# Kernel optimization log

Hardware: AMD Instinct MI355X
Metric: run time of the kernel (lower is better)

The kernel has to match this reference:

```python
import jax, jax.numpy as jnp
import numpy as np

B, E, M, S, D, H = 32, 48, 96, 48, 256, 8  # docs, entities/doc, mentions/doc, sentences/doc, hidden, heads
NEG = -1e9


def _layer_norm(x, g, b, eps=1e-5):
    mu = jnp.mean(x, axis=-1, keepdims=True)
    var = jnp.mean((x - mu) ** 2, axis=-1, keepdims=True)
    return (x - mu) * jax.lax.rsqrt(var + eps) * g + b


def _mha(key_in, value_in, query_in, mask, W, b, ln):
    # W: [4, D, D] = (Wq, Wk, Wv, Wout); b: [4, D]; ln: [2, D] = (gamma, beta)
    Bq, Lq, _ = query_in.shape
    dph = D // H

    def proj(x, i):
        return (x @ W[i] + b[i]).reshape(Bq, -1, H, dph).transpose(0, 2, 1, 3)  # [B,H,L,dph]

    q = proj(query_in, 0)
    k = proj(key_in, 1)
    v = proj(value_in, 2)
    scores = jnp.einsum('bhqd,bhkd->bhqk', q, k) / jnp.sqrt(jnp.float32(dph))
    scores = jnp.where(mask[:, None, :, :], NEG, scores)  # mask True = mention not of this entity
    attn = jax.nn.softmax(scores, axis=-1)
    ctx = jnp.einsum('bhqk,bhkd->bhqd', attn, v).transpose(0, 2, 1, 3).reshape(Bq, Lq, D)
    out = ctx @ W[3] + b[3]
    return _layer_norm(query_in + out, ln[0], ln[1])  # residual + LayerNorm


def _forward(info, entities, mentions, sentences, W1, b1, ln1, W2, b2, ln2):
    # uniform sections -> split_n_pad is an exact reshape
    ent = entities.reshape(B, E, D)
    men = mentions.reshape(B, M, D)
    men_sen = sentences[info[:, 4]].reshape(B, M, D)  # F.embedding(info[:,4], sentences)
    eids = jnp.arange(B * E, dtype=info.dtype).reshape(B, E)  # eid_ranges split per doc
    m_ids = info[:, 0].reshape(B, M)
    index_m = m_ids[:, None, :] != eids[:, :, None]  # [B,E,M], True = masked out
    # head mask varies with row entity i; tail mask varies with column entity j
    mask_h = jnp.broadcast_to(index_m[:, :, None, :], (B, E, E, M)).reshape(B, E * E, M)
    mask_t = jnp.broadcast_to(index_m[:, None, :, :], (B, E, E, M)).reshape(B, E * E, M)
    # meshgrid gather: query_2[b,i,j] = ent[b,j] (c_idx), query_1[b,i,j] = ent[b,i] (r_idx)
    q2 = jnp.broadcast_to(ent[:, None, :, :], (B, E, E, D)).reshape(B, E * E, D)
    q1 = jnp.broadcast_to(ent[:, :, None, :], (B, E, E, D)).reshape(B, E * E, D)
    pair_h = _mha(men_sen, men, q2, mask_h, W1, b1, ln1)
    pair_t = _mha(men_sen, men, q1, mask_t, W2, b2, ln2)
    return pair_h, pair_t


def setup_inputs():
    key = jax.random.key(0)
    ks = jax.random.split(key, 6)
    entities = jax.random.normal(ks[0], (B * E, D), jnp.float32)
    mentions = jax.random.normal(ks[1], (B * M, D), jnp.float32)
    sentences = jax.random.normal(ks[2], (B * S, D), jnp.float32)
    rng = np.random.RandomState(0)
    doc = np.repeat(np.arange(B), M)
    # every entity gets at least one mention (first E mentions per doc), rest random
    eid_local = np.stack([np.concatenate([np.arange(E), rng.randint(0, E, M - E)]) for _ in range(B)]).reshape(-1)
    sid_local = rng.randint(0, S, B * M)
    info = np.zeros((B * M, 6), np.int64)
    info[:, 0] = doc * E + eid_local  # global entity id
    info[:, 4] = doc * S + sid_local  # global sentence id
    section = np.tile(np.array([[E, M]], dtype=np.int64), (B, 1))
    W1 = jax.random.normal(ks[3], (4, D, D), jnp.float32) * 0.05
    W2 = jax.random.normal(ks[4], (4, D, D), jnp.float32) * 0.05
    b1 = jnp.zeros((4, D), jnp.float32)
    b2 = jnp.zeros((4, D), jnp.float32)
    ln1 = jnp.stack([jnp.ones(D), jnp.zeros(D)]).astype(jnp.float32)
    ln2 = jnp.stack([jnp.ones(D), jnp.zeros(D)]).astype(jnp.float32)
    return dict(info=jnp.asarray(info), section=jnp.asarray(section), entities=entities,
                mentions=mentions, sentences=sentences, W1=W1, b1=b1, ln1=ln1, W2=W2, b2=b2, ln2=ln2)


def reference(info, section, entities, mentions, sentences, W1, b1, ln1, W2, b2, ln2):
    return _forward(info, entities, mentions, sentences, W1, b1, ln1, W2, b2, ln2)
```

## Files before the change

kernel.cpp:

```cpp
#include <hip/hip_runtime.h>

#define B_ 32
#define E_ 48
#define M_ 96
#define D_ 256
#define H_ 8
#define DPH_ 32
#define MAXL_ 16
#define JT_ 16
#define RT_ 16
#define RT2_ 8

__global__ __launch_bounds__(256) void build_lists_kernel(
    const int* __restrict__ info, int* __restrict__ cnt, int* __restrict__ lst) {
    int g = blockIdx.x * 256 + threadIdx.x;
    if (g >= B_ * M_) return;
    int e = info[g * 6];
    int pos = atomicAdd(&cnt[e], 1);
    if (pos < MAXL_) lst[e * MAXL_ + pos] = g % M_;
}

__global__ __launch_bounds__(256) void prep_kernel(
    const float* __restrict__ ent, const float* __restrict__ men,
    const float* __restrict__ sen, const int* __restrict__ info,
    const float* __restrict__ W1, const float* __restrict__ b1,
    const float* __restrict__ W2, const float* __restrict__ b2,
    float* __restrict__ qh, float* __restrict__ qt,
    float* __restrict__ k1, float* __restrict__ k2,
    float* __restrict__ u1, float* __restrict__ u2) {
    __shared__ float a[RT_][D_];
    int bx = blockIdx.x;
    int tid = threadIdx.x;
    int type, rg, mha;
    if (bx < 768) { type = 2; rg = bx >> 1; mha = bx & 1; }
    else if (bx < 1152) { type = 1; rg = (bx - 768) >> 1; mha = bx & 1; }
    else { type = 0; rg = (bx - 1152) >> 1; mha = bx & 1; }

    const float* Wb = mha ? W2 : W1;
    const float* bb = mha ? b2 : b1;
    const float* W = Wb + (size_t)type * D_ * D_;
    int tx = tid & 127, ty = tid >> 7;

    if (type == 2) {
        int rowbase = rg * RT2_;
        for (int r = 0; r < RT2_; ++r)
            a[r][tid] = men[(size_t)(rowbase + r) * D_ + tid];
        __syncthreads();

        int r0 = ty * 4;
        float acc0[4], acc1[4];
        {
            float bv0 = bb[2 * D_ + tx], bv1 = bb[2 * D_ + tx + 128];
#pragma unroll
            for (int i = 0; i < 4; ++i) { acc0[i] = bv0; acc1[i] = bv1; }
        }
        for (int k = 0; k < D_; k += 4) {
            float wA0 = W[(size_t)k * D_ + tx],       wB0 = W[(size_t)k * D_ + tx + 128];
            float wA1 = W[(size_t)(k + 1) * D_ + tx], wB1 = W[(size_t)(k + 1) * D_ + tx + 128];
            float wA2 = W[(size_t)(k + 2) * D_ + tx], wB2 = W[(size_t)(k + 2) * D_ + tx + 128];
            float wA3 = W[(size_t)(k + 3) * D_ + tx], wB3 = W[(size_t)(k + 3) * D_ + tx + 128];
#pragma unroll
            for (int i = 0; i < 4; ++i) {
                float4 av = *(const float4*)&a[r0 + i][k];
                acc0[i] = fmaf(av.x, wA0, acc0[i]); acc1[i] = fmaf(av.x, wB0, acc1[i]);
                acc0[i] = fmaf(av.y, wA1, acc0[i]); acc1[i] = fmaf(av.y, wB1, acc1[i]);
                acc0[i] = fmaf(av.z, wA2, acc0[i]); acc1[i] = fmaf(av.z, wB2, acc1[i]);
                acc0[i] = fmaf(av.w, wA3, acc0[i]); acc1[i] = fmaf(av.w, wB3, acc1[i]);
            }
        }
        __syncthreads();
#pragma unroll
        for (int i = 0; i < 4; ++i) {
            a[r0 + i][tx] = acc0[i];
            a[r0 + i][tx + 128] = acc1[i];
        }
        __syncthreads();
        const float* Wo = Wb + (size_t)3 * D_ * D_;
        float* u = mha ? u2 : u1;
        for (int h = 0; h < H_; ++h) {
#pragma unroll
            for (int i = 0; i < 4; ++i) { acc0[i] = 0.f; acc1[i] = 0.f; }
            for (int k = 0; k < DPH_; k += 4) {
                int kk = h * DPH_ + k;
                float wA0 = Wo[(size_t)kk * D_ + tx],       wB0 = Wo[(size_t)kk * D_ + tx + 128];
                float wA1 = Wo[(size_t)(kk + 1) * D_ + tx], wB1 = Wo[(size_t)(kk + 1) * D_ + tx + 128];
                float wA2 = Wo[(size_t)(kk + 2) * D_ + tx], wB2 = Wo[(size_t)(kk + 2) * D_ + tx + 128];
                float wA3 = Wo[(size_t)(kk + 3) * D_ + tx], wB3 = Wo[(size_t)(kk + 3) * D_ + tx + 128];
#pragma unroll
                for (int i = 0; i < 4; ++i) {
                    float4 vv = *(const float4*)&a[r0 + i][kk & 255];
                    acc0[i] = fmaf(vv.x, wA0, acc0[i]); acc1[i] = fmaf(vv.x, wB0, acc1[i]);
                    acc0[i] = fmaf(vv.y, wA1, acc0[i]); acc1[i] = fmaf(vv.y, wB1, acc1[i]);
                    acc0[i] = fmaf(vv.z, wA2, acc0[i]); acc1[i] = fmaf(vv.z, wB2, acc1[i]);
                    acc0[i] = fmaf(vv.w, wA3, acc0[i]); acc1[i] = fmaf(vv.w, wB3, acc1[i]);
                }
            }
#pragma unroll
            for (int i = 0; i < 4; ++i) {
                u[((size_t)(rowbase + r0 + i) * H_ + h) * D_ + tx] = acc0[i];
                u[((size_t)(rowbase + r0 + i) * H_ + h) * D_ + tx + 128] = acc1[i];
            }
        }
        return;
    }

    int rowbase = rg * RT_;
    if (type == 0) {
        for (int r = tid >> 7; r < RT_; r += 2)
            a[r][tid & 127] = ent[(size_t)(rowbase + r) * D_ + (tid & 127)];
        for (int r = tid >> 7; r < RT_; r += 2)
            a[r][(tid & 127) + 128] = ent[(size_t)(rowbase + r) * D_ + (tid & 127) + 128];
    } else {
        for (int r = 0; r < RT_; ++r) {
            int sid = info[(rowbase + r) * 6 + 4];
            a[r][tid] = sen[(size_t)sid * D_ + tid];
        }
    }
    __syncthreads();

    int r0 = ty * 8;
    float acc0[8], acc1[8];
    {
        float bv0 = bb[type * D_ + tx], bv1 = bb[type * D_ + tx + 128];
#pragma unroll
        for (int i = 0; i < 8; ++i) { acc0[i] = bv0; acc1[i] = bv1; }
    }
    for (int k = 0; k < D_; k += 4) {
        float wA0 = W[(size_t)k * D_ + tx],       wB0 = W[(size_t)k * D_ + tx + 128];
        float wA1 = W[(size_t)(k + 1) * D_ + tx], wB1 = W[(size_t)(k + 1) * D_ + tx + 128];
        float wA2 = W[(size_t)(k + 2) * D_ + tx], wB2 = W[(size_t)(k + 2) * D_ + tx + 128];
        float wA3 = W[(size_t)(k + 3) * D_ + tx], wB3 = W[(size_t)(k + 3) * D_ + tx + 128];
#pragma unroll
        for (int i = 0; i < 8; ++i) {
            float4 av = *(const float4*)&a[r0 + i][k];
            acc0[i] = fmaf(av.x, wA0, acc0[i]); acc1[i] = fmaf(av.x, wB0, acc1[i]);
            acc0[i] = fmaf(av.y, wA1, acc0[i]); acc1[i] = fmaf(av.y, wB1, acc1[i]);
            acc0[i] = fmaf(av.z, wA2, acc0[i]); acc1[i] = fmaf(av.z, wB2, acc1[i]);
            acc0[i] = fmaf(av.w, wA3, acc0[i]); acc1[i] = fmaf(av.w, wB3, acc1[i]);
        }
    }

    float* o = (type == 0) ? (mha ? qt : qh) : (mha ? k2 : k1);
#pragma unroll
    for (int i = 0; i < 8; ++i) {
        o[(size_t)(rowbase + r0 + i) * D_ + tx] = acc0[i];
        o[(size_t)(rowbase + r0 + i) * D_ + tx + 128] = acc1[i];
    }
}

__global__ __launch_bounds__(256) void scores_kernel(
    const float* __restrict__ qh, const float* __restrict__ qt,
    const float* __restrict__ k1, const float* __restrict__ k2,
    float* __restrict__ ES) {
    int b = blockIdx.x, h = blockIdx.y, which = blockIdx.z;
    int tid = threadIdx.x;
    const float* q = (which ? qt : qh) + (size_t)b * E_ * D_ + h * DPH_;
    const float* kk = (which ? k2 : k1) + (size_t)b * M_ * D_ + h * DPH_;
    float* ESb = ES + (((size_t)which * B_ + b) * H_ + h) * (M_ * E_);

    __shared__ float qs[E_][DPH_ + 2];
    __shared__ float ks[M_][DPH_ + 2];
    __shared__ float Sb[E_][M_ + 2];
    __shared__ float mx[E_];

    for (int idx = tid; idx < E_ * DPH_; idx += 256) {
        int r = idx >> 5, c = idx & 31;
        qs[r][c] = q[(size_t)r * D_ + c];
    }
    for (int idx = tid; idx < M_ * DPH_; idx += 256) {
        int r = idx >> 5, c = idx & 31;
        ks[r][c] = kk[(size_t)r * D_ + c];
    }
    __syncthreads();
#pragma unroll
    for (int it = 0; it < 18; ++it) {
        int pair = tid + it * 256;
        int qi = pair / 96, m = pair % 96;
        float acc = 0.f;
#pragma unroll
        for (int c = 0; c < DPH_; c += 2) {
            float2 qv = *(const float2*)&qs[qi][c];
            float2 kv = *(const float2*)&ks[m][c];
            acc = fmaf(qv.x, kv.x, acc);
            acc = fmaf(qv.y, kv.y, acc);
        }
        Sb[qi][m] = acc * 0.17677669529663687f;
    }
    __syncthreads();
    if (tid < E_) {
        float mm = -1e30f;
        for (int m = 0; m < M_; ++m) mm = fmaxf(mm, Sb[tid][m]);
        mx[tid] = mm;
    }
    __syncthreads();
    for (int idx = tid; idx < E_ * M_; idx += 256) {
        int qi = idx % E_, m = idx / E_;
        ESb[m * E_ + qi] = __expf(Sb[qi][m] - mx[qi]);
    }
}

__global__ __launch_bounds__(256) void pairs_kernel(
    const int* __restrict__ cnt_arr, const int* __restrict__ lst_arr,
    const float* __restrict__ ES,
    const float* __restrict__ u1, const float* __restrict__ u2,
    const float* __restrict__ ent,
    const float* __restrict__ bo1, const float* __restrict__ bo2,
    const float* __restrict__ ln1, const float* __restrict__ ln2,
    float* __restrict__ out) {
    int tid = threadIdx.x;
    int me = blockIdx.x;
    int b = blockIdx.y;
    int which = blockIdx.z;

    const float* ESb = ES + ((size_t)which * B_ + b) * (H_ * M_ * E_);
    const float* u = which ? u2 : u1;
    const float* bo = which ? bo2 : bo1;
    const float* ln = which ? ln2 : ln1;
    float* outb = out + ((size_t)which * B_ + b) * E_ * E_ * D_;

    __shared__ int lst[MAXL_];
    __shared__ float wj[MAXL_ * H_][JT_];
    __shared__ float dinv_s[H_ * JT_];
    __shared__ float xbuf[JT_][D_ + 4];
    __shared__ int cnt_s;

    if (tid == 0) cnt_s = min(cnt_arr[b * E_ + me], MAXL_);
    if (tid < MAXL_) lst[tid] = lst_arr[(b * E_ + me) * MAXL_ + tid];
    __syncthreads();
    int cnt = cnt_s;
    int K = cnt * H_;

    float bv = bo[tid];
    int wave = tid >> 6, lane = tid & 63;

    for (int j0 = 0; j0 < E_; j0 += JT_) {
        for (int idx = tid; idx < K * 4; idx += 256) {
            int k = idx >> 2, j4 = (idx & 3) * 4;
            int pos = k >> 3, h = k & 7;
            *(float4*)&wj[k][j4] =
                *(const float4*)&ESb[(size_t)(h * M_ + lst[pos]) * E_ + j0 + j4];
        }
        __syncthreads();
        if (tid < H_ * JT_) {
            int h = tid >> 4, j = tid & 15;
            float s = 0.f;
            for (int pos = 0; pos < cnt; ++pos) s += wj[pos * 8 + h][j];
            dinv_s[tid] = 1.0f / s;
        }
        __syncthreads();
        for (int idx = tid; idx < K * JT_; idx += 256) {
            int k = idx >> 4, j = idx & 15;
            wj[k][j] *= dinv_s[((k & 7) << 4) + j];
        }
        __syncthreads();

        float acc[JT_];
#pragma unroll
        for (int j = 0; j < JT_; ++j) acc[j] = 0.f;
        for (int pos = 0; pos < cnt; ++pos) {
            const float* ub = u + (size_t)(b * M_ + lst[pos]) * (H_ * D_) + tid;
#pragma unroll
            for (int h = 0; h < H_; ++h) {
                float uval = ub[(size_t)h * D_];
                const float* wb = wj[pos * 8 + h];
                float4 w0 = *(const float4*)&wb[0];
                float4 w1 = *(const float4*)&wb[4];
                float4 w2 = *(const float4*)&wb[8];
                float4 w3 = *(const float4*)&wb[12];
                acc[0]  = fmaf(w0.x, uval, acc[0]);
                acc[1]  = fmaf(w0.y, uval, acc[1]);
                acc[2]  = fmaf(w0.z, uval, acc[2]);
                acc[3]  = fmaf(w0.w, uval, acc[3]);
                acc[4]  = fmaf(w1.x, uval, acc[4]);
                acc[5]  = fmaf(w1.y, uval, acc[5]);
                acc[6]  = fmaf(w1.z, uval, acc[6]);
                acc[7]  = fmaf(w1.w, uval, acc[7]);
                acc[8]  = fmaf(w2.x, uval, acc[8]);
                acc[9]  = fmaf(w2.y, uval, acc[9]);
                acc[10] = fmaf(w2.z, uval, acc[10]);
                acc[11] = fmaf(w2.w, uval, acc[11]);
                acc[12] = fmaf(w3.x, uval, acc[12]);
                acc[13] = fmaf(w3.y, uval, acc[13]);
                acc[14] = fmaf(w3.z, uval, acc[14]);
                acc[15] = fmaf(w3.w, uval, acc[15]);
            }
        }

#pragma unroll
        for (int j = 0; j < JT_; ++j) {
            float e = ent[(size_t)(b * E_ + j0 + j) * D_ + tid];
            xbuf[j][tid] = e + bv + acc[j];
        }
        __syncthreads();

        for (int jj = wave; jj < JT_; jj += 4) {
            float4 xv = *(const float4*)&xbuf[jj][lane * 4];
            float s = xv.x + xv.y + xv.z + xv.w;
            float sq = xv.x * xv.x + xv.y * xv.y + xv.z * xv.z + xv.w * xv.w;
#pragma unroll
            for (int off = 32; off > 0; off >>= 1) {
                s += __shfl_xor(s, off);
                sq += __shfl_xor(sq, off);
            }
            float mu = s * (1.0f / D_);
            float var = sq * (1.0f / D_) - mu * mu;
            float inv = rsqrtf(fmaxf(var, 0.f) + 1e-5f);
            float4 g = *(const float4*)&ln[lane * 4];
            float4 be = *(const float4*)&ln[D_ + lane * 4];
            float4 y;
            y.x = (xv.x - mu) * inv * g.x + be.x;
            y.y = (xv.y - mu) * inv * g.y + be.y;
            y.z = (xv.z - mu) * inv * g.z + be.z;
            y.w = (xv.w - mu) * inv * g.w + be.w;
            int o = j0 + jj;
            size_t orow = which ? ((size_t)o * E_ + me) : ((size_t)me * E_ + o);
            *(float4*)&outb[orow * D_ + lane * 4] = y;
        }
        __syncthreads();
    }
}

extern "C" void kernel_launch(void* const* d_in, const int* in_sizes, int n_in,
                              void* d_out, int out_size, void* d_ws, size_t ws_size,
                              hipStream_t stream) {
    const int* info = (const int*)d_in[0];
    const float* ent = (const float*)d_in[2];
    const float* men = (const float*)d_in[3];
    const float* sen = (const float*)d_in[4];
    const float* W1 = (const float*)d_in[5];
    const float* b1 = (const float*)d_in[6];
    const float* ln1 = (const float*)d_in[7];
    const float* W2 = (const float*)d_in[8];
    const float* b2 = (const float*)d_in[9];
    const float* ln2 = (const float*)d_in[10];
    float* out = (float*)d_out;

    float* ws = (float*)d_ws;
    size_t off = 0;
    float* qh = ws + off; off += (size_t)B_ * E_ * D_;
    float* qt = ws + off; off += (size_t)B_ * E_ * D_;
    float* k1 = ws + off; off += (size_t)B_ * M_ * D_;
    float* k2 = ws + off; off += (size_t)B_ * M_ * D_;
    float* u1 = ws + off; off += (size_t)B_ * M_ * H_ * D_;
    float* u2 = ws + off; off += (size_t)B_ * M_ * H_ * D_;
    float* ES = ws + off; off += (size_t)2 * B_ * H_ * M_ * E_;
    int* cnt = (int*)(ws + off); off += B_ * E_;
    int* lst = (int*)(ws + off); off += (size_t)B_ * E_ * MAXL_;

    hipMemsetAsync(cnt, 0, B_ * E_ * sizeof(int), stream);
    build_lists_kernel<<<(B_ * M_ + 255) / 256, 256, 0, stream>>>(info, cnt, lst);
    prep_kernel<<<1344, 256, 0, stream>>>(
        ent, men, sen, info, W1, b1, W2, b2, qh, qt, k1, k2, u1, u2);
    scores_kernel<<<dim3(B_, H_, 2), 256, 0, stream>>>(qh, qt, k1, k2, ES);
    pairs_kernel<<<dim3(E_, B_, 2), 256, 0, stream>>>(
        cnt, lst, ES, u1, u2, ent,
        b1 + 3 * D_, b2 + 3 * D_, ln1, ln2, out);
}
```

Measured before the change: 326.4 us.

## Stage weight tiles in shared memory with register prefetch in prep_kernel

The projection GEMMs in prep_kernel now stage 16-row chunks of the weight matrix in a shared-memory buffer. The next chunk is loaded into registers with float4 global loads while the current one is computed, so weights are no longer read from global memory one scalar per k inside the FMA loop. Each thread now owns one output column across all rows of the tile instead of two columns across half the rows. Input rows are loaded with float4. This adds 16 KB of shared memory and a barrier pair per chunk, which may reduce occupancy and add sync overhead.

```diff
diff --git a/kernel.cpp b/kernel.cpp
--- a/kernel.cpp
+++ b/kernel.cpp
@@ -29,6 +29,7 @@
     float* __restrict__ k1, float* __restrict__ k2,
     float* __restrict__ u1, float* __restrict__ u2) {
     __shared__ float a[RT_][D_];
+    __shared__ float ws[16][D_];
     int bx = blockIdx.x;
     int tid = threadIdx.x;
     int type, rg, mha;
@@ -39,113 +40,194 @@
     const float* Wb = mha ? W2 : W1;
     const float* bb = mha ? b2 : b1;
     const float* W = Wb + (size_t)type * D_ * D_;
-    int tx = tid & 127, ty = tid >> 7;
+    int rgp = tid >> 6;
+    int c4w = (tid & 63) * 4;
 
     if (type == 2) {
         int rowbase = rg * RT2_;
-        for (int r = 0; r < RT2_; ++r)
-            a[r][tid] = men[(size_t)(rowbase + r) * D_ + tid];
-        __syncthreads();
-
-        int r0 = ty * 4;
-        float acc0[4], acc1[4];
+#pragma unroll
+        for (int j = 0; j < 2; ++j) {
+            int f = j * 256 + tid;
+            int r = f >> 6, cc = (f & 63) * 4;
+            *(float4*)&a[r][cc] = *(const float4*)&men[(size_t)(rowbase + r) * D_ + cc];
+        }
+        float4 p0 = *(const float4*)&W[(size_t)(0 + rgp) * D_ + c4w];
+        float4 p1 = *(const float4*)&W[(size_t)(4 + rgp) * D_ + c4w];
+        float4 p2 = *(const float4*)&W[(size_t)(8 + rgp) * D_ + c4w];
+        float4 p3 = *(const float4*)&W[(size_t)(12 + rgp) * D_ + c4w];
+        *(float4*)&ws[0 + rgp][c4w] = p0;
+        *(float4*)&ws[4 + rgp][c4w] = p1;
+        *(float4*)&ws[8 + rgp][c4w] = p2;
+        *(float4*)&ws[12 + rgp][c4w] = p3;
+        __syncthreads();
+
+        float acc[8];
         {
-            float bv0 = bb[2 * D_ + tx], bv1 = bb[2 * D_ + tx + 128];
-#pragma unroll
-            for (int i = 0; i < 4; ++i) { acc0[i] = bv0; acc1[i] = bv1; }
-        }
-        for (int k = 0; k < D_; k += 4) {
-            float wA0 = W[(size_t)k * D_ + tx],       wB0 = W[(size_t)k * D_ + tx + 128];
-            float wA1 = W[(size_t)(k + 1) * D_ + tx], wB1 = W[(size_t)(k + 1) * D_ + tx + 128];
-            float wA2 = W[(size_t)(k + 2) * D_ + tx], wB2 = W[(size_t)(k + 2) * D_ + tx + 128];
-            float wA3 = W[(size_t)(k + 3) * D_ + tx], wB3 = W[(size_t)(k + 3) * D_ + tx + 128];
-#pragma unroll
-            for (int i = 0; i < 4; ++i) {
-                float4 av = *(const float4*)&a[r0 + i][k];
-                acc0[i] = fmaf(av.x, wA0, acc0[i]); acc1[i] = fmaf(av.x, wB0, acc1[i]);
-                acc0[i] = fmaf(av.y, wA1, acc0[i]); acc1[i] = fmaf(av.y, wB1, acc1[i]);
-                acc0[i] = fmaf(av.z, wA2, acc0[i]); acc1[i] = fmaf(av.z, wB2, acc1[i]);
-                acc0[i] = fmaf(av.w, wA3, acc0[i]); acc1[i] = fmaf(av.w, wB3, acc1[i]);
-            }
-        }
-        __syncthreads();
-#pragma unroll
-        for (int i = 0; i < 4; ++i) {
-            a[r0 + i][tx] = acc0[i];
-            a[r0 + i][tx + 128] = acc1[i];
-        }
-        __syncthreads();
+            float bv = bb[2 * D_ + tid];
+#pragma unroll
+            for (int r = 0; r < 8; ++r) acc[r] = bv;
+        }
+        for (int c = 0; c < 16; ++c) {
+            int k0 = c << 4;
+            if (c < 15) {
+                const float* Wn = W + (size_t)(k0 + 16) * D_ + c4w;
+                p0 = *(const float4*)(Wn + (size_t)(0 + rgp) * D_);
+                p1 = *(const float4*)(Wn + (size_t)(4 + rgp) * D_);
+                p2 = *(const float4*)(Wn + (size_t)(8 + rgp) * D_);
+                p3 = *(const float4*)(Wn + (size_t)(12 + rgp) * D_);
+            }
+#pragma unroll
+            for (int kk = 0; kk < 16; kk += 4) {
+                float w0 = ws[kk][tid];
+                float w1 = ws[kk + 1][tid];
+                float w2 = ws[kk + 2][tid];
+                float w3 = ws[kk + 3][tid];
+#pragma unroll
+                for (int r = 0; r < 8; ++r) {
+                    float4 xv = *(const float4*)&a[r][k0 + kk];
+                    acc[r] = fmaf(xv.x, w0, acc[r]);
+                    acc[r] = fmaf(xv.y, w1, acc[r]);
+                    acc[r] = fmaf(xv.z, w2, acc[r]);
+                    acc[r] = fmaf(xv.w, w3, acc[r]);
+                }
+            }
+            __syncthreads();
+            if (c < 15) {
+                *(float4*)&ws[0 + rgp][c4w] = p0;
+                *(float4*)&ws[4 + rgp][c4w] = p1;
+                *(float4*)&ws[8 + rgp][c4w] = p2;
+                *(float4*)&ws[12 + rgp][c4w] = p3;
+                __syncthreads();
+            }
+        }
+#pragma unroll
+        for (int r = 0; r < 8; ++r) a[8 + r][tid] = acc[r];
         const float* Wo = Wb + (size_t)3 * D_ * D_;
+        p0 = *(const float4*)&Wo[(size_t)(0 + rgp) * D_ + c4w];
+        p1 = *(const float4*)&Wo[(size_t)(4 + rgp) * D_ + c4w];
+        p2 = *(const float4*)&Wo[(size_t)(8 + rgp) * D_ + c4w];
+        p3 = *(const float4*)&Wo[(size_t)(12 + rgp) * D_ + c4w];
+        *(float4*)&ws[0 + rgp][c4w] = p0;
+        *(float4*)&ws[4 + rgp][c4w] = p1;
+        *(float4*)&ws[8 + rgp][c4w] = p2;
+        *(float4*)&ws[12 + rgp][c4w] = p3;
+        __syncthreads();
+
         float* u = mha ? u2 : u1;
-        for (int h = 0; h < H_; ++h) {
-#pragma unroll
-            for (int i = 0; i < 4; ++i) { acc0[i] = 0.f; acc1[i] = 0.f; }
-            for (int k = 0; k < DPH_; k += 4) {
-                int kk = h * DPH_ + k;
-                float wA0 = Wo[(size_t)kk * D_ + tx],       wB0 = Wo[(size_t)kk * D_ + tx + 128];
-                float wA1 = Wo[(size_t)(kk + 1) * D_ + tx], wB1 = Wo[(size_t)(kk + 1) * D_ + tx + 128];
-                float wA2 = Wo[(size_t)(kk + 2) * D_ + tx], wB2 = Wo[(size_t)(kk + 2) * D_ + tx + 128];
-                float wA3 = Wo[(size_t)(kk + 3) * D_ + tx], wB3 = Wo[(size_t)(kk + 3) * D_ + tx + 128];
-#pragma unroll
-                for (int i = 0; i < 4; ++i) {
-                    float4 vv = *(const float4*)&a[r0 + i][kk & 255];
-                    acc0[i] = fmaf(vv.x, wA0, acc0[i]); acc1[i] = fmaf(vv.x, wB0, acc1[i]);
-                    acc0[i] = fmaf(vv.y, wA1, acc0[i]); acc1[i] = fmaf(vv.y, wB1, acc1[i]);
-                    acc0[i] = fmaf(vv.z, wA2, acc0[i]); acc1[i] = fmaf(vv.z, wB2, acc1[i]);
-                    acc0[i] = fmaf(vv.w, wA3, acc0[i]); acc1[i] = fmaf(vv.w, wB3, acc1[i]);
+        for (int c = 0; c < 16; ++c) {
+            int k0 = c << 4;
+            if (c < 15) {
+                const float* Wn = Wo + (size_t)(k0 + 16) * D_ + c4w;
+                p0 = *(const float4*)(Wn + (size_t)(0 + rgp) * D_);
+                p1 = *(const float4*)(Wn + (size_t)(4 + rgp) * D_);
+                p2 = *(const float4*)(Wn + (size_t)(8 + rgp) * D_);
+                p3 = *(const float4*)(Wn + (size_t)(12 + rgp) * D_);
+            }
+            if ((c & 1) == 0) {
+#pragma unroll
+                for (int r = 0; r < 8; ++r) acc[r] = 0.f;
+            }
+#pragma unroll
+            for (int kk = 0; kk < 16; kk += 4) {
+                float w0 = ws[kk][tid];
+                float w1 = ws[kk + 1][tid];
+                float w2 = ws[kk + 2][tid];
+                float w3 = ws[kk + 3][tid];
+#pragma unroll
+                for (int r = 0; r < 8; ++r) {
+                    float4 xv = *(const float4*)&a[8 + r][k0 + kk];
+                    acc[r] = fmaf(xv.x, w0, acc[r]);
+                    acc[r] = fmaf(xv.y, w1, acc[r]);
+                    acc[r] = fmaf(xv.z, w2, acc[r]);
+                    acc[r] = fmaf(xv.w, w3, acc[r]);
                 }
             }
-#pragma unroll
-            for (int i = 0; i < 4; ++i) {
-                u[((size_t)(rowbase + r0 + i) * H_ + h) * D_ + tx] = acc0[i];
-                u[((size_t)(rowbase + r0 + i) * H_ + h) * D_ + tx + 128] = acc1[i];
+            if (c & 1) {
+                int h = c >> 1;
+#pragma unroll
+                for (int r = 0; r < 8; ++r)
+                    u[((size_t)(rowbase + r) * H_ + h) * D_ + tid] = acc[r];
+            }
+            __syncthreads();
+            if (c < 15) {
+                *(float4*)&ws[0 + rgp][c4w] = p0;
+                *(float4*)&ws[4 + rgp][c4w] = p1;
+                *(float4*)&ws[8 + rgp][c4w] = p2;
+                *(float4*)&ws[12 + rgp][c4w] = p3;
+                __syncthreads();
             }
         }
         return;
     }
 
     int rowbase = rg * RT_;
-    if (type == 0) {
-        for (int r = tid >> 7; r < RT_; r += 2)
-            a[r][tid & 127] = ent[(size_t)(rowbase + r) * D_ + (tid & 127)];
-        for (int r = tid >> 7; r < RT_; r += 2)
-            a[r][(tid & 127) + 128] = ent[(size_t)(rowbase + r) * D_ + (tid & 127) + 128];
-    } else {
-        for (int r = 0; r < RT_; ++r) {
+#pragma unroll
+    for (int j = 0; j < 4; ++j) {
+        int f = j * 256 + tid;
+        int r = f >> 6, cc = (f & 63) * 4;
+        const float* src;
+        if (type == 0) {
+            src = &ent[(size_t)(rowbase + r) * D_ + cc];
+        } else {
             int sid = info[(rowbase + r) * 6 + 4];
-            a[r][tid] = sen[(size_t)sid * D_ + tid];
-        }
-    }
+            src = &sen[(size_t)sid * D_ + cc];
+        }
+        *(float4*)&a[r][cc] = *(const float4*)src;
+    }
+    float4 p0 = *(const float4*)&W[(size_t)(0 + rgp) * D_ + c4w];
+    float4 p1 = *(const float4*)&W[(size_t)(4 + rgp) * D_ + c4w];
+    float4 p2 = *(const float4*)&W[(size_t)(8 + rgp) * D_ + c4w];
+    float4 p3 = *(const float4*)&W[(size_t)(12 + rgp) * D_ + c4w];
+    *(float4*)&ws[0 + rgp][c4w] = p0;
+    *(float4*)&ws[4 + rgp][c4w] = p1;
+    *(float4*)&ws[8 + rgp][c4w] = p2;
+    *(float4*)&ws[12 + rgp][c4w] = p3;
     __syncthreads();
 
-    int r0 = ty * 8;
-    float acc0[8], acc1[8];
+    float acc[16];
     {
-        float bv0 = bb[type * D_ + tx], bv1 = bb[type * D_ + tx + 128];
-#pragma unroll
-        for (int i = 0; i < 8; ++i) { acc0[i] = bv0; acc1[i] = bv1; }
-    }
-    for (int k = 0; k < D_; k += 4) {
-        float wA0 = W[(size_t)k * D_ + tx],       wB0 = W[(size_t)k * D_ + tx + 128];
-        float wA1 = W[(size_t)(k + 1) * D_ + tx], wB1 = W[(size_t)(k + 1) * D_ + tx + 128];
-        float wA2 = W[(size_t)(k + 2) * D_ + tx], wB2 = W[(size_t)(k + 2) * D_ + tx + 128];
-        float wA3 = W[(size_t)(k + 3) * D_ + tx], wB3 = W[(size_t)(k + 3) * D_ + tx + 128];
-#pragma unroll
-        for (int i = 0; i < 8; ++i) {
-            float4 av = *(const float4*)&a[r0 + i][k];
-            acc0[i] = fmaf(av.x, wA0, acc0[i]); acc1[i] = fmaf(av.x, wB0, acc1[i]);
-            acc0[i] = fmaf(av.y, wA1, acc0[i]); acc1[i] = fmaf(av.y, wB1, acc1[i]);
-            acc0[i] = fmaf(av.z, wA2, acc0[i]); acc1[i] = fmaf(av.z, wB2, acc1[i]);
-            acc0[i] = fmaf(av.w, wA3, acc0[i]); acc1[i] = fmaf(av.w, wB3, acc1[i]);
+        float bv = bb[type * D_ + tid];
+#pragma unroll
+        for (int r = 0; r < 16; ++r) acc[r] = bv;
+    }
+    for (int c = 0; c < 16; ++c) {
+        int k0 = c << 4;
+        if (c < 15) {
+            const float* Wn = W + (size_t)(k0 + 16) * D_ + c4w;
+            p0 = *(const float4*)(Wn + (size_t)(0 + rgp) * D_);
+            p1 = *(const float4*)(Wn + (size_t)(4 + rgp) * D_);
+            p2 = *(const float4*)(Wn + (size_t)(8 + rgp) * D_);
+            p3 = *(const float4*)(Wn + (size_t)(12 + rgp) * D_);
+        }
+#pragma unroll
+        for (int kk = 0; kk < 16; kk += 4) {
+            float w0 = ws[kk][tid];
+            float w1 = ws[kk + 1][tid];
+            float w2 = ws[kk + 2][tid];
+            float w3 = ws[kk + 3][tid];
+#pragma unroll
+            for (int r = 0; r < 16; ++r) {
+                float4 xv = *(const float4*)&a[r][k0 + kk];
+                acc[r] = fmaf(xv.x, w0, acc[r]);
+                acc[r] = fmaf(xv.y, w1, acc[r]);
+                acc[r] = fmaf(xv.z, w2, acc[r]);
+                acc[r] = fmaf(xv.w, w3, acc[r]);
+            }
+        }
+        __syncthreads();
+        if (c < 15) {
+            *(float4*)&ws[0 + rgp][c4w] = p0;
+            *(float4*)&ws[4 + rgp][c4w] = p1;
+            *(float4*)&ws[8 + rgp][c4w] = p2;
+            *(float4*)&ws[12 + rgp][c4w] = p3;
+            __syncthreads();
         }
     }
 
     float* o = (type == 0) ? (mha ? qt : qh) : (mha ? k2 : k1);
 #pragma unroll
-    for (int i = 0; i < 8; ++i) {
-        o[(size_t)(rowbase + r0 + i) * D_ + tx] = acc0[i];
-        o[(size_t)(rowbase + r0 + i) * D_ + tx + 128] = acc1[i];
-    }
+    for (int r = 0; r < 16; ++r)
+        o[(size_t)(rowbase + r) * D_ + tid] = acc[r];
 }
 
 __global__ __launch_bounds__(256) void scores_kernel(
```

Result: slower. 350.0 us (+7.2%).

## Project keys per sentence instead of per mention and fold list building into prep

Applied to the files above, without the earlier changes.

The key projection now runs over the 48 unique sentences per document instead of the 96 gathered mention-sentence rows, and the scores kernel looks up each mention's sentence index to pick its key row. This halves the key-projection GEMM blocks and the key workspace. The separate list-building kernel is merged into the first 12 blocks of the prep kernel, which removes one launch. It assumes sentence ids are local to each document (b*S offset).

```diff
diff --git a/kernel.cpp b/kernel.cpp
--- a/kernel.cpp
+++ b/kernel.cpp
@@ -3,6 +3,7 @@
 #define B_ 32
 #define E_ 48
 #define M_ 96
+#define S_ 48
 #define D_ 256
 #define H_ 8
 #define DPH_ 32
@@ -11,15 +12,6 @@
 #define RT_ 16
 #define RT2_ 8
 
-__global__ __launch_bounds__(256) void build_lists_kernel(
-    const int* __restrict__ info, int* __restrict__ cnt, int* __restrict__ lst) {
-    int g = blockIdx.x * 256 + threadIdx.x;
-    if (g >= B_ * M_) return;
-    int e = info[g * 6];
-    int pos = atomicAdd(&cnt[e], 1);
-    if (pos < MAXL_) lst[e * MAXL_ + pos] = g % M_;
-}
-
 __global__ __launch_bounds__(256) void prep_kernel(
     const float* __restrict__ ent, const float* __restrict__ men,
     const float* __restrict__ sen, const int* __restrict__ info,
@@ -27,14 +19,23 @@
     const float* __restrict__ W2, const float* __restrict__ b2,
     float* __restrict__ qh, float* __restrict__ qt,
     float* __restrict__ k1, float* __restrict__ k2,
-    float* __restrict__ u1, float* __restrict__ u2) {
+    float* __restrict__ u1, float* __restrict__ u2,
+    int* __restrict__ cnt, int* __restrict__ lst) {
     __shared__ float a[RT_][D_];
     int bx = blockIdx.x;
     int tid = threadIdx.x;
+
+    if (bx < 12) {
+        int g = bx * 256 + tid;
+        int e = info[g * 6];
+        int pos = atomicAdd(&cnt[e], 1);
+        if (pos < MAXL_) lst[e * MAXL_ + pos] = g % M_;
+    }
+
     int type, rg, mha;
     if (bx < 768) { type = 2; rg = bx >> 1; mha = bx & 1; }
-    else if (bx < 1152) { type = 1; rg = (bx - 768) >> 1; mha = bx & 1; }
-    else { type = 0; rg = (bx - 1152) >> 1; mha = bx & 1; }
+    else if (bx < 960) { type = 1; rg = (bx - 768) >> 1; mha = bx & 1; }
+    else { type = 0; rg = (bx - 960) >> 1; mha = bx & 1; }
 
     const float* Wb = mha ? W2 : W1;
     const float* bb = mha ? b2 : b1;
@@ -111,10 +112,8 @@
         for (int r = tid >> 7; r < RT_; r += 2)
             a[r][(tid & 127) + 128] = ent[(size_t)(rowbase + r) * D_ + (tid & 127) + 128];
     } else {
-        for (int r = 0; r < RT_; ++r) {
-            int sid = info[(rowbase + r) * 6 + 4];
-            a[r][tid] = sen[(size_t)sid * D_ + tid];
-        }
+        for (int r = 0; r < RT_; ++r)
+            a[r][tid] = sen[(size_t)(rowbase + r) * D_ + tid];
     }
     __syncthreads();
 
@@ -151,36 +150,40 @@
 __global__ __launch_bounds__(256) void scores_kernel(
     const float* __restrict__ qh, const float* __restrict__ qt,
     const float* __restrict__ k1, const float* __restrict__ k2,
+    const int* __restrict__ info,
     float* __restrict__ ES) {
     int b = blockIdx.x, h = blockIdx.y, which = blockIdx.z;
     int tid = threadIdx.x;
     const float* q = (which ? qt : qh) + (size_t)b * E_ * D_ + h * DPH_;
-    const float* kk = (which ? k2 : k1) + (size_t)b * M_ * D_ + h * DPH_;
+    const float* kk = (which ? k2 : k1) + (size_t)b * S_ * D_ + h * DPH_;
     float* ESb = ES + (((size_t)which * B_ + b) * H_ + h) * (M_ * E_);
 
     __shared__ float qs[E_][DPH_ + 2];
-    __shared__ float ks[M_][DPH_ + 2];
+    __shared__ float ks[S_][DPH_ + 2];
     __shared__ float Sb[E_][M_ + 2];
     __shared__ float mx[E_];
+    __shared__ int sidl[M_];
 
     for (int idx = tid; idx < E_ * DPH_; idx += 256) {
         int r = idx >> 5, c = idx & 31;
         qs[r][c] = q[(size_t)r * D_ + c];
     }
-    for (int idx = tid; idx < M_ * DPH_; idx += 256) {
+    for (int idx = tid; idx < S_ * DPH_; idx += 256) {
         int r = idx >> 5, c = idx & 31;
         ks[r][c] = kk[(size_t)r * D_ + c];
     }
+    if (tid < M_) sidl[tid] = info[(b * M_ + tid) * 6 + 4] - b * S_;
     __syncthreads();
 #pragma unroll
     for (int it = 0; it < 18; ++it) {
         int pair = tid + it * 256;
         int qi = pair / 96, m = pair % 96;
+        int sr = sidl[m];
         float acc = 0.f;
 #pragma unroll
         for (int c = 0; c < DPH_; c += 2) {
             float2 qv = *(const float2*)&qs[qi][c];
-            float2 kv = *(const float2*)&ks[m][c];
+            float2 kv = *(const float2*)&ks[sr][c];
             acc = fmaf(qv.x, kv.x, acc);
             acc = fmaf(qv.y, kv.y, acc);
         }
@@ -339,8 +342,8 @@
     size_t off = 0;
     float* qh = ws + off; off += (size_t)B_ * E_ * D_;
     float* qt = ws + off; off += (size_t)B_ * E_ * D_;
-    float* k1 = ws + off; off += (size_t)B_ * M_ * D_;
-    float* k2 = ws + off; off += (size_t)B_ * M_ * D_;
+    float* k1 = ws + off; off += (size_t)B_ * S_ * D_;
+    float* k2 = ws + off; off += (size_t)B_ * S_ * D_;
     float* u1 = ws + off; off += (size_t)B_ * M_ * H_ * D_;
     float* u2 = ws + off; off += (size_t)B_ * M_ * H_ * D_;
     float* ES = ws + off; off += (size_t)2 * B_ * H_ * M_ * E_;
@@ -348,10 +351,9 @@
     int* lst = (int*)(ws + off); off += (size_t)B_ * E_ * MAXL_;
 
     hipMemsetAsync(cnt, 0, B_ * E_ * sizeof(int), stream);
-    build_lists_kernel<<<(B_ * M_ + 255) / 256, 256, 0, stream>>>(info, cnt, lst);
-    prep_kernel<<<1344, 256, 0, stream>>>(
-        ent, men, sen, info, W1, b1, W2, b2, qh, qt, k1, k2, u1, u2);
-    scores_kernel<<<dim3(B_, H_, 2), 256, 0, stream>>>(qh, qt, k1, k2, ES);
+    prep_kernel<<<1152, 256, 0, stream>>>(
+        ent, men, sen, info, W1, b1, W2, b2, qh, qt, k1, k2, u1, u2, cnt, lst);
+    scores_kernel<<<dim3(B_, H_, 2), 256, 0, stream>>>(qh, qt, k1, k2, info, ES);
     pairs_kernel<<<dim3(E_, B_, 2), 256, 0, stream>>>(
         cnt, lst, ES, u1, u2, ent,
         b1 + 3 * D_, b2 + 3 * D_, ln1, ln2, out);
```

New measurement: 312.2 us. -4.3%, faster.
